# Kernel tuning notes

Measured on AMD Instinct MI355X. Metric: run time of the kernel, lower is better.

## Reference

```python
import jax, jax.numpy as jnp
import numpy as np

B, T, C, H = 128, 256, 512, 512

def setup_inputs() -> dict:
    key = jax.random.key(0)
    k1, k2, k3, k4 = jax.random.split(key, 4)
    x = jax.random.normal(k1, (B, T, C), dtype=jnp.float32)
    # nn.Linear(n_embed, H_size, bias=False).weight has shape [H, C]; scaled init
    s = 1.0 / np.sqrt(C)
    Wq = jax.random.normal(k2, (H, C), dtype=jnp.float32) * s
    Wk = jax.random.normal(k3, (H, C), dtype=jnp.float32) * s
    Wv = jax.random.normal(k4, (H, C), dtype=jnp.float32) * s
    return {"x": x, "Wq": Wq, "Wk": Wk, "Wv": Wv}

def reference(x, Wq, Wk, Wv):
    # q,k,v: [B,T,H] = x @ W.T (torch Linear convention)
    q = jnp.einsum('btc,hc->bth', x, Wq)
    k = jnp.einsum('btc,hc->bth', x, Wk)
    v = jnp.einsum('btc,hc->bth', x, Wv)
    scale = k.shape[-1] ** -0.5
    score = jnp.einsum('bqh,bkh->bqk', q, k) * scale  # [B,T,T]
    # causal mask: position j attends to i only if i <= j
    i = jnp.arange(T)
    causal = i[None, :] <= i[:, None]  # [T,T] lower-triangular
    score = jnp.where(causal[None, :, :], score, -jnp.inf)
    attn = jax.nn.softmax(score, axis=-1)
    # dropout is identity in eval mode
    out = jnp.einsum('bqk,bkh->bqh', attn, v)  # [B,T,H]
    return out
```

## Files before the change

kernel.cpp:

```cpp
#include <hip/hip_runtime.h>

#define B_ 128
#define T_ 256
#define C_ 512
#define H_ 512
#define CSCALE 0.063763824f

typedef _Float16 f16x8 __attribute__((ext_vector_type(8)));
typedef _Float16 f16x4 __attribute__((ext_vector_type(4)));
typedef float    f32x4 __attribute__((ext_vector_type(4)));

__device__ __forceinline__ void gld16(const void* gsrc, void* ldst) {
  __builtin_amdgcn_global_load_lds(
      (__attribute__((address_space(1))) void*)gsrc,
      (__attribute__((address_space(3))) void*)ldst, 16, 0, 0);
}

__global__ __launch_bounds__(256) void cvt_kernel(
    const float4* __restrict__ x, const float4* __restrict__ wq,
    const float4* __restrict__ wk, const float4* __restrict__ wv,
    f16x4* __restrict__ dst) {
  const int NX = (B_ * T_ * C_) / 4;
  const int NW = (H_ * C_) / 4;
  const int total = NX + 3 * NW;
  int gid = blockIdx.x * 256 + threadIdx.x;
  int gsz = gridDim.x * 256;
  for (int i = gid; i < total; i += gsz) {
    float4 f;
    if (i < NX)            f = x[i];
    else if (i < NX + NW)  f = wq[i - NX];
    else if (i < NX + 2*NW) f = wk[i - NX - NW];
    else                   f = wv[i - NX - 2*NW];
    f16x4 u = {(_Float16)f.x, (_Float16)f.y, (_Float16)f.z, (_Float16)f.w};
    dst[i] = u;
  }
}

__global__ __launch_bounds__(256) void proj_kernel(
    const _Float16* __restrict__ xh, const _Float16* __restrict__ wh,
    _Float16* __restrict__ qh, _Float16* __restrict__ kh,
    _Float16* __restrict__ vth) {
  __shared__ _Float16 As[128 * 32];
  __shared__ _Float16 Bs[128 * 32];

  const int tid  = threadIdx.x;
  const int lane = tid & 63;
  const int wave = tid >> 6;
  const int lr = lane & 15, lk = lane >> 4;
  const int m0 = blockIdx.x * 128;
  const int n0 = blockIdx.y * 128;
  const int z  = blockIdx.z;
  const _Float16* wz = wh + z * (H_ * C_);

  const int wm = (wave >> 1) * 64;
  const int wn = (wave & 1) * 64;

  f32x4 acc[4][4];
#pragma unroll
  for (int i = 0; i < 4; ++i)
#pragma unroll
    for (int j = 0; j < 4; ++j) acc[i][j] = {0.f, 0.f, 0.f, 0.f};

  const int srow = tid >> 2, scol = (tid & 3) * 8;
  const _Float16* aSrc = xh + (m0 + srow) * C_ + scol;
  const _Float16* bSrc = wz + (n0 + srow) * C_ + scol;

  for (int k0 = 0; k0 < C_; k0 += 32) {
    __syncthreads();
#pragma unroll
    for (int i = 0; i < 2; ++i) {
      gld16((const void*)(aSrc + i * 64 * C_ + k0), (void*)&As[i * 2048 + wave * 512]);
      gld16((const void*)(bSrc + i * 64 * C_ + k0), (void*)&Bs[i * 2048 + wave * 512]);
    }
    __syncthreads();

    f16x8 a[4], b[4];
#pragma unroll
    for (int mi = 0; mi < 4; ++mi)
      a[mi] = *(const f16x8*)&As[(wm + mi * 16 + lr) * 32 + lk * 8];
#pragma unroll
    for (int ni = 0; ni < 4; ++ni)
      b[ni] = *(const f16x8*)&Bs[(wn + ni * 16 + lr) * 32 + lk * 8];
#pragma unroll
    for (int mi = 0; mi < 4; ++mi)
#pragma unroll
      for (int ni = 0; ni < 4; ++ni)
        acc[mi][ni] = __builtin_amdgcn_mfma_f32_16x16x32_f16(a[mi], b[ni], acc[mi][ni], 0, 0, 0);
  }

  if (z < 2) {
    _Float16* out = (z == 0) ? qh : kh;
#pragma unroll
    for (int mi = 0; mi < 4; ++mi) {
      int mbase = m0 + wm + mi * 16 + lk * 4;
#pragma unroll
      for (int ni = 0; ni < 4; ++ni) {
        int n = n0 + wn + ni * 16 + lr;
#pragma unroll
        for (int r = 0; r < 4; ++r)
          out[(mbase + r) * H_ + n] = (_Float16)acc[mi][ni][r];
      }
    }
  } else {
#pragma unroll
    for (int mi = 0; mi < 4; ++mi) {
      int mbase = m0 + wm + mi * 16 + lk * 4;
      int bb = mbase >> 8, tt = mbase & 255;
#pragma unroll
      for (int ni = 0; ni < 4; ++ni) {
        int n = n0 + wn + ni * 16 + lr;
        f16x4 u = {(_Float16)acc[mi][ni][0], (_Float16)acc[mi][ni][1],
                   (_Float16)acc[mi][ni][2], (_Float16)acc[mi][ni][3]};
        *(f16x4*)&vth[bb * (H_ * T_) + n * T_ + tt] = u;
      }
    }
  }
}

__global__ __launch_bounds__(256, 2) void attn_kernel(
    const _Float16* __restrict__ qh, const _Float16* __restrict__ kh,
    const _Float16* __restrict__ vth, float* __restrict__ dout) {
  __shared__ _Float16 Ks[16384];
  __shared__ _Float16 Vs[16384];

  const int tid  = threadIdx.x;
  const int lane = tid & 63;
  const int wq   = tid >> 6;
  const int lr = lane & 15, lk = lane >> 4;
  const int qt = blockIdx.x;
  const int b  = blockIdx.y;
  const int q0 = qt * 64;
  const int nkv = (qt + 1) * 2;

  f16x8 qf[16];
  const _Float16* qrow = qh + (b * T_ + q0 + wq * 16 + lr) * H_;
#pragma unroll
  for (int f = 0; f < 16; ++f) qf[f] = *(const f16x8*)&qrow[f * 32 + lk * 8];

  f32x4 o[32];
#pragma unroll
  for (int i = 0; i < 32; ++i) o[i] = {0.f, 0.f, 0.f, 0.f};
  float m[4], l[4];
#pragma unroll
  for (int r = 0; r < 4; ++r) { m[r] = -1e30f; l[r] = 0.f; }

  for (int kvt = 0; kvt < nkv; ++kvt) {
    const int kv0 = kvt * 32;
    __syncthreads();
#pragma unroll
    for (int i = 0; i < 8; ++i) {
      int c = i * 256 + tid;
      {
        int hb = c >> 5, kv = c & 31;
        gld16((const void*)(kh + (b * T_ + kv0 + kv) * H_ + hb * 8),
              (void*)&Ks[i * 2048 + wq * 512]);
      }
      {
        int tb = c >> 9, h = c & 511;
        gld16((const void*)(vth + (b * H_ + h) * T_ + kv0 + tb * 8),
              (void*)&Vs[i * 2048 + wq * 512]);
      }
    }
    __syncthreads();

    f32x4 s0 = {0.f, 0.f, 0.f, 0.f}, s1 = {0.f, 0.f, 0.f, 0.f};
#pragma unroll
    for (int ks = 0; ks < 16; ++ks) {
      f16x8 b0 = *(const f16x8*)&Ks[((ks * 4 + lk) * 32 + lr) * 8];
      f16x8 b1 = *(const f16x8*)&Ks[((ks * 4 + lk) * 32 + 16 + lr) * 8];
      s0 = __builtin_amdgcn_mfma_f32_16x16x32_f16(qf[ks], b0, s0, 0, 0, 0);
      s1 = __builtin_amdgcn_mfma_f32_16x16x32_f16(qf[ks], b1, s1, 0, 0, 0);
    }

    float p0[4], p1[4], rm[4];
    const int rowb = q0 + wq * 16 + lk * 4;
#pragma unroll
    for (int r = 0; r < 4; ++r) {
      float v0 = (kv0 + lr      > rowb + r) ? -1e30f : s0[r];
      float v1 = (kv0 + 16 + lr > rowb + r) ? -1e30f : s1[r];
      s0[r] = v0; s1[r] = v1;
      rm[r] = fmaxf(v0, v1);
    }
#pragma unroll
    for (int off = 1; off < 16; off <<= 1)
#pragma unroll
      for (int r = 0; r < 4; ++r) rm[r] = fmaxf(rm[r], __shfl_xor(rm[r], off, 64));

    bool need = false;
#pragma unroll
    for (int r = 0; r < 4; ++r) need = need || (rm[r] > m[r] + 64.f);
    if (__any(need)) {
#pragma unroll
      for (int r = 0; r < 4; ++r) {
        float mn = fmaxf(m[r], rm[r]);
        float al = __builtin_amdgcn_exp2f((m[r] - mn) * CSCALE);
        m[r] = mn; l[r] *= al;
#pragma unroll
        for (int hf = 0; hf < 32; ++hf) o[hf][r] *= al;
      }
    }

    float rs[4];
#pragma unroll
    for (int r = 0; r < 4; ++r) {
      p0[r] = __builtin_amdgcn_exp2f((s0[r] - m[r]) * CSCALE);
      p1[r] = __builtin_amdgcn_exp2f((s1[r] - m[r]) * CSCALE);
      rs[r] = p0[r] + p1[r];
    }
#pragma unroll
    for (int off = 1; off < 16; off <<= 1)
#pragma unroll
      for (int r = 0; r < 4; ++r) rs[r] += __shfl_xor(rs[r], off, 64);
#pragma unroll
    for (int r = 0; r < 4; ++r) l[r] += rs[r];

    __syncthreads();

    _Float16* Ps = &Ks[wq * 512];
#pragma unroll
    for (int r = 0; r < 4; ++r) {
      Ps[(lk * 4 + r) * 32 + lr]      = (_Float16)p0[r];
      Ps[(lk * 4 + r) * 32 + 16 + lr] = (_Float16)p1[r];
    }
    f16x8 pa = *(const f16x8*)&Ps[lr * 32 + lk * 8];

#pragma unroll
    for (int hf = 0; hf < 32; ++hf) {
      f16x8 vb = *(const f16x8*)&Vs[(lk * 512 + hf * 16 + lr) * 8];
      o[hf] = __builtin_amdgcn_mfma_f32_16x16x32_f16(pa, vb, o[hf], 0, 0, 0);
    }
  }

  float linv[4];
#pragma unroll
  for (int r = 0; r < 4; ++r) linv[r] = 1.0f / l[r];
  float* orow = dout + (size_t)(b * T_ + q0 + wq * 16 + lk * 4) * H_;
#pragma unroll
  for (int hf = 0; hf < 32; ++hf)
#pragma unroll
    for (int r = 0; r < 4; ++r)
      orow[(size_t)r * H_ + hf * 16 + lr] = o[hf][r] * linv[r];
}

extern "C" void kernel_launch(void* const* d_in, const int* in_sizes, int n_in,
                              void* d_out, int out_size, void* d_ws, size_t ws_size,
                              hipStream_t stream) {
  const size_t NXE = (size_t)B_ * T_ * C_;
  const size_t NWE = (size_t)3 * H_ * C_;
  const size_t NQE = (size_t)B_ * T_ * H_;
  const size_t need = (NXE + NWE + 3 * NQE) * sizeof(_Float16);
  if (ws_size < need) return;

  const float* x  = (const float*)d_in[0];
  const float* wq = (const float*)d_in[1];
  const float* wk = (const float*)d_in[2];
  const float* wv = (const float*)d_in[3];

  _Float16* xh  = (_Float16*)d_ws;
  _Float16* wh  = xh + NXE;
  _Float16* qh  = wh + NWE;
  _Float16* kh  = qh + NQE;
  _Float16* vth = kh + NQE;

  cvt_kernel<<<2048, 256, 0, stream>>>((const float4*)x, (const float4*)wq,
                                       (const float4*)wk, (const float4*)wv,
                                       (f16x4*)xh);
  proj_kernel<<<dim3(256, 4, 3), dim3(256), 0, stream>>>(xh, wh, qh, kh, vth);
  attn_kernel<<<dim3(4, 128), dim3(256), 0, stream>>>(qh, kh, vth, (float*)d_out);
}
```

Measured before the change: 197.0 us.

## Restructure attention into independent 16-row waves with balanced causal pairing and direct K/V loads

Attention now runs one 16-query-row tile per wave, two waves per block. Each block pairs a short causal tile with a long one (p and 15-p) to balance work, and the grid grows to 8x128 blocks of 128 threads. K and V are read straight from global memory (through cache) instead of being staged in LDS, which removes the block-wide barriers and the 64KB shared buffers. The QK loop splits its accumulation into two chains for more MFMA overlap, and the P buffer is padded to avoid LDS bank conflicts. The cost is more redundant global/L2 traffic for K and V, since waves no longer share loaded tiles.

```diff
diff --git a/kernel.cpp b/kernel.cpp
--- a/kernel.cpp
+++ b/kernel.cpp
@@ -117,23 +117,23 @@
   }
 }
 
-__global__ __launch_bounds__(256, 2) void attn_kernel(
+__global__ __launch_bounds__(128) void attn_kernel(
     const _Float16* __restrict__ qh, const _Float16* __restrict__ kh,
     const _Float16* __restrict__ vth, float* __restrict__ dout) {
-  __shared__ _Float16 Ks[16384];
-  __shared__ _Float16 Vs[16384];
+  __shared__ _Float16 Ps[2 * 16 * 40];
 
   const int tid  = threadIdx.x;
   const int lane = tid & 63;
   const int wq   = tid >> 6;
   const int lr = lane & 15, lk = lane >> 4;
-  const int qt = blockIdx.x;
+  const int p  = blockIdx.x;
   const int b  = blockIdx.y;
-  const int q0 = qt * 64;
-  const int nkv = (qt + 1) * 2;
+  const int qw = wq ? (15 - p) : p;
+  const int q0 = qw * 16;
+  const int nkv = (qw >> 1) + 1;
 
   f16x8 qf[16];
-  const _Float16* qrow = qh + (b * T_ + q0 + wq * 16 + lr) * H_;
+  const _Float16* qrow = qh + ((size_t)b * T_ + q0 + lr) * H_;
 #pragma unroll
   for (int f = 0; f < 16; ++f) qf[f] = *(const f16x8*)&qrow[f * 32 + lk * 8];
 
@@ -144,36 +144,33 @@
 #pragma unroll
   for (int r = 0; r < 4; ++r) { m[r] = -1e30f; l[r] = 0.f; }
 
+  const _Float16* kbase = kh + (size_t)b * T_ * H_;
+  const _Float16* vbase = vth + (size_t)b * H_ * T_;
+  _Float16* Pw = &Ps[wq * 640];
+
   for (int kvt = 0; kvt < nkv; ++kvt) {
     const int kv0 = kvt * 32;
-    __syncthreads();
-#pragma unroll
-    for (int i = 0; i < 8; ++i) {
-      int c = i * 256 + tid;
-      {
-        int hb = c >> 5, kv = c & 31;
-        gld16((const void*)(kh + (b * T_ + kv0 + kv) * H_ + hb * 8),
-              (void*)&Ks[i * 2048 + wq * 512]);
-      }
-      {
-        int tb = c >> 9, h = c & 511;
-        gld16((const void*)(vth + (b * H_ + h) * T_ + kv0 + tb * 8),
-              (void*)&Vs[i * 2048 + wq * 512]);
-      }
-    }
-    __syncthreads();
 
     f32x4 s0 = {0.f, 0.f, 0.f, 0.f}, s1 = {0.f, 0.f, 0.f, 0.f};
-#pragma unroll
-    for (int ks = 0; ks < 16; ++ks) {
-      f16x8 b0 = *(const f16x8*)&Ks[((ks * 4 + lk) * 32 + lr) * 8];
-      f16x8 b1 = *(const f16x8*)&Ks[((ks * 4 + lk) * 32 + 16 + lr) * 8];
+    f32x4 t0 = {0.f, 0.f, 0.f, 0.f}, t1 = {0.f, 0.f, 0.f, 0.f};
+    const _Float16* krow0 = kbase + (size_t)(kv0 + lr) * H_ + lk * 8;
+    const _Float16* krow1 = krow0 + 16 * H_;
+#pragma unroll
+    for (int ks = 0; ks < 16; ks += 2) {
+      f16x8 b0 = *(const f16x8*)&krow0[ks * 32];
+      f16x8 b1 = *(const f16x8*)&krow1[ks * 32];
+      f16x8 c0 = *(const f16x8*)&krow0[ks * 32 + 32];
+      f16x8 c1 = *(const f16x8*)&krow1[ks * 32 + 32];
       s0 = __builtin_amdgcn_mfma_f32_16x16x32_f16(qf[ks], b0, s0, 0, 0, 0);
       s1 = __builtin_amdgcn_mfma_f32_16x16x32_f16(qf[ks], b1, s1, 0, 0, 0);
-    }
+      t0 = __builtin_amdgcn_mfma_f32_16x16x32_f16(qf[ks + 1], c0, t0, 0, 0, 0);
+      t1 = __builtin_amdgcn_mfma_f32_16x16x32_f16(qf[ks + 1], c1, t1, 0, 0, 0);
+    }
+    s0 = s0 + t0;
+    s1 = s1 + t1;
 
     float p0[4], p1[4], rm[4];
-    const int rowb = q0 + wq * 16 + lk * 4;
+    const int rowb = q0 + lk * 4;
 #pragma unroll
     for (int r = 0; r < 4; ++r) {
       float v0 = (kv0 + lr      > rowb + r) ? -1e30f : s0[r];
@@ -214,19 +211,17 @@
 #pragma unroll
     for (int r = 0; r < 4; ++r) l[r] += rs[r];
 
-    __syncthreads();
-
-    _Float16* Ps = &Ks[wq * 512];
 #pragma unroll
     for (int r = 0; r < 4; ++r) {
-      Ps[(lk * 4 + r) * 32 + lr]      = (_Float16)p0[r];
-      Ps[(lk * 4 + r) * 32 + 16 + lr] = (_Float16)p1[r];
-    }
-    f16x8 pa = *(const f16x8*)&Ps[lr * 32 + lk * 8];
-
+      Pw[(lk * 4 + r) * 40 + lr]      = (_Float16)p0[r];
+      Pw[(lk * 4 + r) * 40 + 16 + lr] = (_Float16)p1[r];
+    }
+    f16x8 pa = *(const f16x8*)&Pw[lr * 40 + lk * 8];
+
+    const _Float16* vcol = vbase + (size_t)lr * T_ + kv0 + lk * 8;
 #pragma unroll
     for (int hf = 0; hf < 32; ++hf) {
-      f16x8 vb = *(const f16x8*)&Vs[(lk * 512 + hf * 16 + lr) * 8];
+      f16x8 vb = *(const f16x8*)&vcol[(size_t)hf * 16 * T_];
       o[hf] = __builtin_amdgcn_mfma_f32_16x16x32_f16(pa, vb, o[hf], 0, 0, 0);
     }
   }
@@ -234,7 +229,7 @@
   float linv[4];
 #pragma unroll
   for (int r = 0; r < 4; ++r) linv[r] = 1.0f / l[r];
-  float* orow = dout + (size_t)(b * T_ + q0 + wq * 16 + lk * 4) * H_;
+  float* orow = dout + ((size_t)b * T_ + q0 + lk * 4) * H_;
 #pragma unroll
   for (int hf = 0; hf < 32; ++hf)
 #pragma unroll
@@ -266,5 +261,5 @@
                                        (const float4*)wk, (const float4*)wv,
                                        (f16x4*)xh);
   proj_kernel<<<dim3(256, 4, 3), dim3(256), 0, stream>>>(xh, wh, qh, kh, vth);
-  attn_kernel<<<dim3(4, 128), dim3(256), 0, stream>>>(qh, kh, vth, (float*)d_out);
-}
+  attn_kernel<<<dim3(8, 128), dim3(128), 0, stream>>>(qh, kh, vth, (float*)d_out);
+}
```

Measured after the change: 238.0 us. 20.8% more time.

## Split fused flash attention into QK GEMM, softmax, and PV GEMM kernels

Applied to the files above, without the earlier changes.

Replaces the single fused online-softmax attention kernel with three kernels: a tiled QK^T GEMM over the causal lower-triangle tiles that writes fp16 scores into the reused x workspace, a row-wise softmax kernel, and a tiled PV GEMM limited to the causal K range. The conversion kernel is also split into separate x and weight kernels. The aim is to replace the fused kernel, which had few blocks and heavy register pressure, with regular 128x128 MFMA GEMM tiles that give more parallelism. The cost is writing and re-reading the full score matrix, extra launches, and rounding the normalized probabilities to fp16.

```diff
diff --git a/kernel.cpp b/kernel.cpp
--- a/kernel.cpp
+++ b/kernel.cpp
@@ -16,24 +16,27 @@
       (__attribute__((address_space(3))) void*)ldst, 16, 0, 0);
 }
 
-__global__ __launch_bounds__(256) void cvt_kernel(
-    const float4* __restrict__ x, const float4* __restrict__ wq,
-    const float4* __restrict__ wk, const float4* __restrict__ wv,
-    f16x4* __restrict__ dst) {
+__global__ __launch_bounds__(256) void cvtx_kernel(
+    const float4* __restrict__ x, f16x4* __restrict__ dst) {
   const int NX = (B_ * T_ * C_) / 4;
-  const int NW = (H_ * C_) / 4;
-  const int total = NX + 3 * NW;
   int gid = blockIdx.x * 256 + threadIdx.x;
   int gsz = gridDim.x * 256;
-  for (int i = gid; i < total; i += gsz) {
-    float4 f;
-    if (i < NX)            f = x[i];
-    else if (i < NX + NW)  f = wq[i - NX];
-    else if (i < NX + 2*NW) f = wk[i - NX - NW];
-    else                   f = wv[i - NX - 2*NW];
+  for (int i = gid; i < NX; i += gsz) {
+    float4 f = x[i];
     f16x4 u = {(_Float16)f.x, (_Float16)f.y, (_Float16)f.z, (_Float16)f.w};
     dst[i] = u;
   }
+}
+
+__global__ __launch_bounds__(256) void cvtw_kernel(
+    const float4* __restrict__ wq, const float4* __restrict__ wk,
+    const float4* __restrict__ wv, f16x4* __restrict__ dst) {
+  const int NW = (H_ * C_) / 4;
+  int i = blockIdx.x * 256 + threadIdx.x;
+  if (i >= 3 * NW) return;
+  float4 f = (i < NW) ? wq[i] : (i < 2 * NW ? wk[i - NW] : wv[i - 2 * NW]);
+  f16x4 u = {(_Float16)f.x, (_Float16)f.y, (_Float16)f.z, (_Float16)f.w};
+  dst[i] = u;
 }
 
 __global__ __launch_bounds__(256) void proj_kernel(
@@ -62,8 +65,8 @@
     for (int j = 0; j < 4; ++j) acc[i][j] = {0.f, 0.f, 0.f, 0.f};
 
   const int srow = tid >> 2, scol = (tid & 3) * 8;
-  const _Float16* aSrc = xh + (m0 + srow) * C_ + scol;
-  const _Float16* bSrc = wz + (n0 + srow) * C_ + scol;
+  const _Float16* aSrc = xh + (size_t)(m0 + srow) * C_ + scol;
+  const _Float16* bSrc = wz + (size_t)(n0 + srow) * C_ + scol;
 
   for (int k0 = 0; k0 < C_; k0 += 32) {
     __syncthreads();
@@ -98,7 +101,7 @@
         int n = n0 + wn + ni * 16 + lr;
 #pragma unroll
         for (int r = 0; r < 4; ++r)
-          out[(mbase + r) * H_ + n] = (_Float16)acc[mi][ni][r];
+          out[(size_t)(mbase + r) * H_ + n] = (_Float16)acc[mi][ni][r];
       }
     }
   } else {
@@ -111,135 +114,174 @@
         int n = n0 + wn + ni * 16 + lr;
         f16x4 u = {(_Float16)acc[mi][ni][0], (_Float16)acc[mi][ni][1],
                    (_Float16)acc[mi][ni][2], (_Float16)acc[mi][ni][3]};
-        *(f16x4*)&vth[bb * (H_ * T_) + n * T_ + tt] = u;
+        *(f16x4*)&vth[(size_t)bb * (H_ * T_) + (size_t)n * T_ + tt] = u;
       }
     }
   }
 }
 
-__global__ __launch_bounds__(256, 2) void attn_kernel(
+__global__ __launch_bounds__(256) void qk_kernel(
     const _Float16* __restrict__ qh, const _Float16* __restrict__ kh,
-    const _Float16* __restrict__ vth, float* __restrict__ dout) {
-  __shared__ _Float16 Ks[16384];
-  __shared__ _Float16 Vs[16384];
+    _Float16* __restrict__ S) {
+  __shared__ _Float16 As[128 * 32];
+  __shared__ _Float16 Bs[128 * 32];
 
   const int tid  = threadIdx.x;
   const int lane = tid & 63;
-  const int wq   = tid >> 6;
+  const int wave = tid >> 6;
   const int lr = lane & 15, lk = lane >> 4;
-  const int qt = blockIdx.x;
+  const int tx = blockIdx.x;
+  const int ti = (tx + 1) >> 1, tj = tx >> 1;
   const int b  = blockIdx.y;
-  const int q0 = qt * 64;
-  const int nkv = (qt + 1) * 2;
-
-  f16x8 qf[16];
-  const _Float16* qrow = qh + (b * T_ + q0 + wq * 16 + lr) * H_;
-#pragma unroll
-  for (int f = 0; f < 16; ++f) qf[f] = *(const f16x8*)&qrow[f * 32 + lk * 8];
-
-  f32x4 o[32];
-#pragma unroll
-  for (int i = 0; i < 32; ++i) o[i] = {0.f, 0.f, 0.f, 0.f};
-  float m[4], l[4];
-#pragma unroll
-  for (int r = 0; r < 4; ++r) { m[r] = -1e30f; l[r] = 0.f; }
-
-  for (int kvt = 0; kvt < nkv; ++kvt) {
-    const int kv0 = kvt * 32;
-    __syncthreads();
-#pragma unroll
-    for (int i = 0; i < 8; ++i) {
-      int c = i * 256 + tid;
-      {
-        int hb = c >> 5, kv = c & 31;
-        gld16((const void*)(kh + (b * T_ + kv0 + kv) * H_ + hb * 8),
-              (void*)&Ks[i * 2048 + wq * 512]);
-      }
-      {
-        int tb = c >> 9, h = c & 511;
-        gld16((const void*)(vth + (b * H_ + h) * T_ + kv0 + tb * 8),
-              (void*)&Vs[i * 2048 + wq * 512]);
-      }
-    }
-    __syncthreads();
-
-    f32x4 s0 = {0.f, 0.f, 0.f, 0.f}, s1 = {0.f, 0.f, 0.f, 0.f};
-#pragma unroll
-    for (int ks = 0; ks < 16; ++ks) {
-      f16x8 b0 = *(const f16x8*)&Ks[((ks * 4 + lk) * 32 + lr) * 8];
-      f16x8 b1 = *(const f16x8*)&Ks[((ks * 4 + lk) * 32 + 16 + lr) * 8];
-      s0 = __builtin_amdgcn_mfma_f32_16x16x32_f16(qf[ks], b0, s0, 0, 0, 0);
-      s1 = __builtin_amdgcn_mfma_f32_16x16x32_f16(qf[ks], b1, s1, 0, 0, 0);
-    }
-
-    float p0[4], p1[4], rm[4];
-    const int rowb = q0 + wq * 16 + lk * 4;
-#pragma unroll
-    for (int r = 0; r < 4; ++r) {
-      float v0 = (kv0 + lr      > rowb + r) ? -1e30f : s0[r];
-      float v1 = (kv0 + 16 + lr > rowb + r) ? -1e30f : s1[r];
-      s0[r] = v0; s1[r] = v1;
-      rm[r] = fmaxf(v0, v1);
-    }
-#pragma unroll
-    for (int off = 1; off < 16; off <<= 1)
-#pragma unroll
-      for (int r = 0; r < 4; ++r) rm[r] = fmaxf(rm[r], __shfl_xor(rm[r], off, 64));
-
-    bool need = false;
-#pragma unroll
-    for (int r = 0; r < 4; ++r) need = need || (rm[r] > m[r] + 64.f);
-    if (__any(need)) {
-#pragma unroll
-      for (int r = 0; r < 4; ++r) {
-        float mn = fmaxf(m[r], rm[r]);
-        float al = __builtin_amdgcn_exp2f((m[r] - mn) * CSCALE);
-        m[r] = mn; l[r] *= al;
-#pragma unroll
-        for (int hf = 0; hf < 32; ++hf) o[hf][r] *= al;
-      }
-    }
-
-    float rs[4];
-#pragma unroll
-    for (int r = 0; r < 4; ++r) {
-      p0[r] = __builtin_amdgcn_exp2f((s0[r] - m[r]) * CSCALE);
-      p1[r] = __builtin_amdgcn_exp2f((s1[r] - m[r]) * CSCALE);
-      rs[r] = p0[r] + p1[r];
-    }
-#pragma unroll
-    for (int off = 1; off < 16; off <<= 1)
-#pragma unroll
-      for (int r = 0; r < 4; ++r) rs[r] += __shfl_xor(rs[r], off, 64);
-#pragma unroll
-    for (int r = 0; r < 4; ++r) l[r] += rs[r];
-
-    __syncthreads();
-
-    _Float16* Ps = &Ks[wq * 512];
-#pragma unroll
-    for (int r = 0; r < 4; ++r) {
-      Ps[(lk * 4 + r) * 32 + lr]      = (_Float16)p0[r];
-      Ps[(lk * 4 + r) * 32 + 16 + lr] = (_Float16)p1[r];
-    }
-    f16x8 pa = *(const f16x8*)&Ps[lr * 32 + lk * 8];
-
-#pragma unroll
-    for (int hf = 0; hf < 32; ++hf) {
-      f16x8 vb = *(const f16x8*)&Vs[(lk * 512 + hf * 16 + lr) * 8];
-      o[hf] = __builtin_amdgcn_mfma_f32_16x16x32_f16(pa, vb, o[hf], 0, 0, 0);
-    }
-  }
-
-  float linv[4];
-#pragma unroll
-  for (int r = 0; r < 4; ++r) linv[r] = 1.0f / l[r];
-  float* orow = dout + (size_t)(b * T_ + q0 + wq * 16 + lk * 4) * H_;
-#pragma unroll
-  for (int hf = 0; hf < 32; ++hf)
-#pragma unroll
-    for (int r = 0; r < 4; ++r)
-      orow[(size_t)r * H_ + hf * 16 + lr] = o[hf][r] * linv[r];
+  const int m0 = ti * 128, n0 = tj * 128;
+
+  const int wm = (wave >> 1) * 64;
+  const int wn = (wave & 1) * 64;
+
+  f32x4 acc[4][4];
+#pragma unroll
+  for (int i = 0; i < 4; ++i)
+#pragma unroll
+    for (int j = 0; j < 4; ++j) acc[i][j] = {0.f, 0.f, 0.f, 0.f};
+
+  const int srow = tid >> 2, scol = (tid & 3) * 8;
+  const _Float16* aSrc = qh + ((size_t)b * T_ + m0 + srow) * H_ + scol;
+  const _Float16* bSrc = kh + ((size_t)b * T_ + n0 + srow) * H_ + scol;
+
+  for (int k0 = 0; k0 < H_; k0 += 32) {
+    __syncthreads();
+#pragma unroll
+    for (int i = 0; i < 2; ++i) {
+      gld16((const void*)(aSrc + i * 64 * H_ + k0), (void*)&As[i * 2048 + wave * 512]);
+      gld16((const void*)(bSrc + i * 64 * H_ + k0), (void*)&Bs[i * 2048 + wave * 512]);
+    }
+    __syncthreads();
+
+    f16x8 a[4], b4[4];
+#pragma unroll
+    for (int mi = 0; mi < 4; ++mi)
+      a[mi] = *(const f16x8*)&As[(wm + mi * 16 + lr) * 32 + lk * 8];
+#pragma unroll
+    for (int ni = 0; ni < 4; ++ni)
+      b4[ni] = *(const f16x8*)&Bs[(wn + ni * 16 + lr) * 32 + lk * 8];
+#pragma unroll
+    for (int mi = 0; mi < 4; ++mi)
+#pragma unroll
+      for (int ni = 0; ni < 4; ++ni)
+        acc[mi][ni] = __builtin_amdgcn_mfma_f32_16x16x32_f16(a[mi], b4[ni], acc[mi][ni], 0, 0, 0);
+  }
+
+  _Float16* sb = S + (size_t)b * T_ * T_;
+#pragma unroll
+  for (int mi = 0; mi < 4; ++mi) {
+    int mbase = m0 + wm + mi * 16 + lk * 4;
+#pragma unroll
+    for (int ni = 0; ni < 4; ++ni) {
+      int n = n0 + wn + ni * 16 + lr;
+#pragma unroll
+      for (int r = 0; r < 4; ++r)
+        sb[(size_t)(mbase + r) * T_ + n] = (_Float16)acc[mi][ni][r];
+    }
+  }
+}
+
+__global__ __launch_bounds__(256) void sm_kernel(_Float16* __restrict__ S) {
+  const int tid  = threadIdx.x;
+  const int lane = tid & 63;
+  const int wave = tid >> 6;
+  const int R = blockIdx.x * 4 + wave;
+  const int b = R >> 8, i = R & 255;
+
+  _Float16* row = S + ((size_t)b * T_ + i) * T_ + lane * 4;
+  f16x4 v4 = *(const f16x4*)row;
+  float v[4];
+  float m = -1e30f;
+#pragma unroll
+  for (int e = 0; e < 4; ++e) {
+    int j = lane * 4 + e;
+    v[e] = (j > i) ? -1e30f : (float)v4[e];
+    m = fmaxf(m, v[e]);
+  }
+#pragma unroll
+  for (int off = 1; off < 64; off <<= 1) m = fmaxf(m, __shfl_xor(m, off, 64));
+  float s = 0.f;
+#pragma unroll
+  for (int e = 0; e < 4; ++e) {
+    v[e] = (v[e] <= -1e30f) ? 0.f : __builtin_amdgcn_exp2f((v[e] - m) * CSCALE);
+    s += v[e];
+  }
+#pragma unroll
+  for (int off = 1; off < 64; off <<= 1) s += __shfl_xor(s, off, 64);
+  float li = 1.0f / s;
+  f16x4 o = {(_Float16)(v[0] * li), (_Float16)(v[1] * li),
+             (_Float16)(v[2] * li), (_Float16)(v[3] * li)};
+  *(f16x4*)row = o;
+}
+
+__global__ __launch_bounds__(256) void pv_kernel(
+    const _Float16* __restrict__ P, const _Float16* __restrict__ vth,
+    float* __restrict__ dout) {
+  __shared__ _Float16 As[128 * 32];
+  __shared__ _Float16 Bs[128 * 32];
+
+  const int tid  = threadIdx.x;
+  const int lane = tid & 63;
+  const int wave = tid >> 6;
+  const int lr = lane & 15, lk = lane >> 4;
+  const int ti = blockIdx.x;
+  const int m0 = ti * 128;
+  const int n0 = blockIdx.y * 128;
+  const int b  = blockIdx.z;
+  const int kmax = (ti + 1) * 128;
+
+  const int wm = (wave >> 1) * 64;
+  const int wn = (wave & 1) * 64;
+
+  f32x4 acc[4][4];
+#pragma unroll
+  for (int i = 0; i < 4; ++i)
+#pragma unroll
+    for (int j = 0; j < 4; ++j) acc[i][j] = {0.f, 0.f, 0.f, 0.f};
+
+  const int srow = tid >> 2, scol = (tid & 3) * 8;
+  const _Float16* aSrc = P + ((size_t)b * T_ + m0 + srow) * T_ + scol;
+  const _Float16* bSrc = vth + ((size_t)b * H_ + n0 + srow) * T_ + scol;
+
+  for (int k0 = 0; k0 < kmax; k0 += 32) {
+    __syncthreads();
+#pragma unroll
+    for (int i = 0; i < 2; ++i) {
+      gld16((const void*)(aSrc + i * 64 * T_ + k0), (void*)&As[i * 2048 + wave * 512]);
+      gld16((const void*)(bSrc + i * 64 * T_ + k0), (void*)&Bs[i * 2048 + wave * 512]);
+    }
+    __syncthreads();
+
+    f16x8 a[4], b4[4];
+#pragma unroll
+    for (int mi = 0; mi < 4; ++mi)
+      a[mi] = *(const f16x8*)&As[(wm + mi * 16 + lr) * 32 + lk * 8];
+#pragma unroll
+    for (int ni = 0; ni < 4; ++ni)
+      b4[ni] = *(const f16x8*)&Bs[(wn + ni * 16 + lr) * 32 + lk * 8];
+#pragma unroll
+    for (int mi = 0; mi < 4; ++mi)
+#pragma unroll
+      for (int ni = 0; ni < 4; ++ni)
+        acc[mi][ni] = __builtin_amdgcn_mfma_f32_16x16x32_f16(a[mi], b4[ni], acc[mi][ni], 0, 0, 0);
+  }
+
+  float* ob = dout + (size_t)b * T_ * H_;
+#pragma unroll
+  for (int mi = 0; mi < 4; ++mi) {
+    int mbase = m0 + wm + mi * 16 + lk * 4;
+#pragma unroll
+    for (int ni = 0; ni < 4; ++ni) {
+      int n = n0 + wn + ni * 16 + lr;
+#pragma unroll
+      for (int r = 0; r < 4; ++r)
+        ob[(size_t)(mbase + r) * H_ + n] = acc[mi][ni][r];
+    }
+  }
 }
 
 extern "C" void kernel_launch(void* const* d_in, const int* in_sizes, int n_in,
@@ -257,14 +299,17 @@
   const float* wv = (const float*)d_in[3];
 
   _Float16* xh  = (_Float16*)d_ws;
-  _Float16* wh  = xh + NXE;
-  _Float16* qh  = wh + NWE;
+  _Float16* whh = xh + NXE;
+  _Float16* qh  = whh + NWE;
   _Float16* kh  = qh + NQE;
   _Float16* vth = kh + NQE;
-
-  cvt_kernel<<<2048, 256, 0, stream>>>((const float4*)x, (const float4*)wq,
-                                       (const float4*)wk, (const float4*)wv,
-                                       (f16x4*)xh);
-  proj_kernel<<<dim3(256, 4, 3), dim3(256), 0, stream>>>(xh, wh, qh, kh, vth);
-  attn_kernel<<<dim3(4, 128), dim3(256), 0, stream>>>(qh, kh, vth, (float*)d_out);
-}
+  _Float16* S   = xh;
+
+  cvtx_kernel<<<2048, 256, 0, stream>>>((const float4*)x, (f16x4*)xh);
+  cvtw_kernel<<<768, 256, 0, stream>>>((const float4*)wq, (const float4*)wk,
+                                       (const float4*)wv, (f16x4*)whh);
+  proj_kernel<<<dim3(256, 4, 3), dim3(256), 0, stream>>>(xh, whh, qh, kh, vth);
+  qk_kernel<<<dim3(3, 128), dim3(256), 0, stream>>>(qh, kh, S);
+  sm_kernel<<<8192, 256, 0, stream>>>(S);
+  pv_kernel<<<dim3(2, 4, 128), dim3(256), 0, stream>>>(S, vth, (float*)d_out);
+}
```

Result: faster. 162.0 us (-17.8%).
